# Kernel optimization log

Measured on AMD Instinct MI355X. Metric: run time of the kernel, lower is better.

Reference implementation:

```python
import jax, jax.numpy as jnp
import numpy as np

DIM = 768
NUM_HEADS = 12
HEAD_DIM = DIM // NUM_HEADS
SCALE = HEAD_DIM ** -0.5
B, N = 16, 640  # N = 8*8 + 24*24


def setup_inputs() -> dict:
    key = jax.random.key(0)
    ks = jax.random.split(key, 4)
    x = jax.random.normal(ks[0], (B, N, DIM), dtype=jnp.float32)
    # weights stored input-major: y = x @ W + b (equiv. to torch Linear with W = weight.T)
    qkv_w = jax.random.normal(ks[1], (DIM, 3 * DIM), dtype=jnp.float32) * (DIM ** -0.5)
    qkv_b = jnp.zeros((3 * DIM,), dtype=jnp.float32)
    proj_w = jax.random.normal(ks[2], (DIM, DIM), dtype=jnp.float32) * (DIM ** -0.5)
    proj_b = jnp.zeros((DIM,), dtype=jnp.float32)
    w = jnp.ones((2,), dtype=jnp.float32)
    return {"x": x, "qkv_w": qkv_w, "qkv_b": qkv_b, "proj_w": proj_w,
            "proj_b": proj_b, "w": w, "t_h": 8, "t_w": 8, "s_h": 24, "s_w": 24}


def reference(x, qkv_w, qkv_b, proj_w, proj_b, w, t_h, t_w, s_h, s_w):
    b, n, c = x.shape
    qkv = (x @ qkv_w + qkv_b).reshape(b, n, 3, NUM_HEADS, HEAD_DIM)
    qkv = jnp.transpose(qkv, (2, 0, 3, 1, 4))  # [3, B, H, N, D]
    q, k, v = qkv[0], qkv[1], qkv[2]
    attn = jnp.einsum('bhnd,bhmd->bhnm', q, k) * SCALE  # [B,H,N,N]
    attn0 = jax.nn.softmax(attn, axis=-1)
    attn1 = jnp.square(jax.nn.relu(attn))
    ws = jax.nn.softmax(w)  # exp(w_i)/sum(exp(w)) blend weights
    attn = attn0 * ws[0] + attn1 * ws[1]
    out = jnp.einsum('bhnm,bhmd->bhnd', attn, v)  # [B,H,N,D]
    out = jnp.transpose(out, (0, 2, 1, 3)).reshape(b, n, c)
    return out @ proj_w + proj_b
```

## Files before the change

kernel.cpp:

```cpp
#include <hip/hip_runtime.h>
#include <hip/hip_bf16.h>

typedef __attribute__((ext_vector_type(8))) short short8;
typedef __attribute__((ext_vector_type(4))) float floatx4;
typedef __hip_bfloat16 bf16;

#define DIM 768
#define NH 12
#define HD 64
#define BB 16
#define NN 640
#define BH (BB*NH)
#define MROWS (BB*NN)
#define QKVN (3*DIM)
#define SCALE 0.125f

__device__ __forceinline__ floatx4 mfma16(short8 a, short8 b, floatx4 c) {
    return __builtin_amdgcn_mfma_f32_16x16x32_bf16(a, b, c, 0, 0, 0);
}

__device__ __forceinline__ void async_ld16(const bf16* g, bf16* l) {
    __builtin_amdgcn_global_load_lds(
        (const __attribute__((address_space(1))) void*)g,
        (__attribute__((address_space(3))) void*)l, 16, 0, 0);
}

__device__ __forceinline__ unsigned pack_bf2(float a, float b) {
    union { bf16 h; unsigned short u; } x, y;
    x.h = __float2bfloat16(a); y.h = __float2bfloat16(b);
    return (unsigned)x.u | ((unsigned)y.u << 16);
}


__global__ void cvt_x(const float* __restrict__ x, bf16* __restrict__ xb, int n4) {
    int i = blockIdx.x * blockDim.x + threadIdx.x;
    if (i >= n4) return;
    float4 v = ((const float4*)x)[i];
    bf16* p = xb + (size_t)i * 4;
    p[0] = __float2bfloat16(v.x);
    p[1] = __float2bfloat16(v.y);
    p[2] = __float2bfloat16(v.z);
    p[3] = __float2bfloat16(v.w);
}

__global__ void tr_cvt(const float* __restrict__ src, bf16* __restrict__ dst, int R, int C) {
    __shared__ float tile[32][33];
    int bx = blockIdx.x, by = blockIdx.y;
    int tx = threadIdx.x, ty = threadIdx.y;
    for (int j = 0; j < 4; ++j)
        tile[ty + j*8][tx] = src[(size_t)(by*32 + ty + j*8) * C + bx*32 + tx];
    __syncthreads();
    for (int j = 0; j < 4; ++j)
        dst[(size_t)(bx*32 + ty + j*8) * R + by*32 + tx] = __float2bfloat16(tile[tx][ty + j*8]);
}

__global__ void v_tr(const bf16* __restrict__ qkv, bf16* __restrict__ vT) {
    __shared__ bf16 tile[32][33];
    int bhc = blockIdx.z;
    int b = bhc / NH, h = bhc - b * NH;
    int tt = blockIdx.x, dt = blockIdx.y;
    int tx = threadIdx.x, ty = threadIdx.y;
    for (int j = 0; j < 4; ++j) {
        int tok = tt*32 + ty + j*8;
        tile[ty + j*8][tx] = qkv[(size_t)(b*NN + tok)*QKVN + 2*DIM + h*HD + dt*32 + tx];
    }
    __syncthreads();
    for (int j = 0; j < 4; ++j) {
        int d = dt*32 + ty + j*8;
        vT[((size_t)bhc*HD + d)*NN + tt*32 + tx] = tile[tx][ty + j*8];
    }
}

template<int MODE>
__global__ __launch_bounds__(256) void gemm_bt(
    const bf16* __restrict__ A, const bf16* __restrict__ B, const float* __restrict__ bias,
    int M, int N, int K,
    bf16* __restrict__ outb, float* __restrict__ outf)
{
    __shared__ __align__(16) bf16 As[128*32];
    __shared__ __align__(16) bf16 Bs[128*32];

    const int t = threadIdx.x;
    const int lane = t & 63, wave = t >> 6;
    const int l15 = lane & 15, quad = lane >> 4;
    const int wm = (wave >> 1) * 64, wn = (wave & 1) * 64;
    const int m0 = blockIdx.x * 128, n0 = blockIdx.y * 128;

    floatx4 acc[4][4];
    floatx4 zero = {0.f, 0.f, 0.f, 0.f};
    for (int i = 0; i < 4; ++i)
        for (int j = 0; j < 4; ++j)
            acc[i][j] = zero;

    for (int kk = 0; kk < K; kk += 32) {
        __syncthreads();
        for (int s = 0; s < 2; ++s) {
            int cid = s * 256 + t;
            int row = cid >> 2;
            int c8  = (cid & 3) << 3;
            int lbase = (s * 256 + wave * 64) * 8;
            async_ld16(A + (size_t)(m0 + row) * K + kk + c8, As + lbase);
            async_ld16(B + (size_t)(n0 + row) * K + kk + c8, Bs + lbase);
        }
        __syncthreads();
        short8 af[4], bfv[4];
        for (int fm = 0; fm < 4; ++fm)
            af[fm] = *(const short8*)(As + (wm + fm*16 + l15) * 32 + quad * 8);
        for (int fn = 0; fn < 4; ++fn)
            bfv[fn] = *(const short8*)(Bs + (wn + fn*16 + l15) * 32 + quad * 8);
        for (int fm = 0; fm < 4; ++fm)
            for (int fn = 0; fn < 4; ++fn)
                acc[fm][fn] = mfma16(af[fm], bfv[fn], acc[fm][fn]);
    }

    for (int fm = 0; fm < 4; ++fm) {
        for (int fn = 0; fn < 4; ++fn) {
            int n = n0 + wn + fn*16 + l15;
            float bn = bias[n];
            for (int r = 0; r < 4; ++r) {
                int m = m0 + wm + fm*16 + quad*4 + r;
                float v = acc[fm][fn][r] + bn;
                if (MODE == 0) {
                    if (n < DIM) v *= SCALE;
                    outb[(size_t)m * N + n] = __float2bfloat16(v);
                } else {
                    outf[(size_t)m * N + n] = v;
                }
            }
        }
    }
}

__global__ __launch_bounds__(256) void attn_kernel(
    const bf16* __restrict__ qkv, const bf16* __restrict__ vT,
    const float* __restrict__ w2, bf16* __restrict__ ao)
{
    const int bh = blockIdx.y;
    const int b = bh / NH, h = bh - b * NH;
    const int t = threadIdx.x;
    const int wave = t >> 6;
    const int lane = t & 63;
    const int l15 = lane & 15, quad = lane >> 4;
    const int qrow0 = blockIdx.x * 64 + wave * 16;

    float w0 = w2[0], w1 = w2[1];
    float wmx = fmaxf(w0, w1);
    float e0 = __expf(w0 - wmx), e1 = __expf(w1 - wmx);
    float ws0 = e0 / (e0 + e1), ws1 = 1.0f - ws0;

    __shared__ __align__(16) bf16 Kb[2][32*64];
    __shared__ __align__(16) bf16 Vb[2][64*32];
    __shared__ __align__(16) bf16 Ps[4][16*40];
    __shared__ __align__(16) bf16 Pr[4][16*40];

    const bf16* kg = qkv + (size_t)(b*NN)*QKVN + DIM + h*HD;
    const bf16* vg = vT + (size_t)bh * HD * NN;

    const bf16* qrow = qkv + (size_t)(b*NN + qrow0 + l15) * QKVN + h*HD;
    short8 aq0 = *(const short8*)(qrow + quad*8);
    short8 aq1 = *(const short8*)(qrow + 32 + quad*8);

    const int krow = t >> 3;
    const int kcg  = ((t & 7) ^ (krow & 7)) * 8;
    const int vrow = t >> 2;
    const int vcg  = (t & 3) * 8;

    async_ld16(kg + (size_t)krow * QKVN + kcg, &Kb[0][wave*512]);
    async_ld16(vg + (size_t)vrow * NN + vcg,   &Vb[0][wave*512]);

    floatx4 zero = {0.f, 0.f, 0.f, 0.f};
    floatx4 accS[4], accR[4];
    for (int i = 0; i < 4; ++i) { accS[i] = zero; accR[i] = zero; }
    float lsum = 0.f;

    const int chLo = (quad ^ (l15 & 7)) * 8;
    const int chHi = chLo ^ 32;

    for (int kt = 0; kt < 20; ++kt) {
        const int cur = kt & 1;
        __syncthreads();
        if (kt + 1 < 20) {
            async_ld16(kg + (size_t)((kt+1)*32 + krow) * QKVN + kcg, &Kb[cur^1][wave*512]);
            async_ld16(vg + (size_t)vrow * NN + (kt+1)*32 + vcg,     &Vb[cur^1][wave*512]);
        }

        const bf16* Kc = Kb[cur];
        short8 ak0lo = *(const short8*)(Kc + l15*64 + chLo);
        short8 ak0hi = *(const short8*)(Kc + l15*64 + chHi);
        short8 ak1lo = *(const short8*)(Kc + (16 + l15)*64 + chLo);
        short8 ak1hi = *(const short8*)(Kc + (16 + l15)*64 + chHi);

        const bf16* Vc = Vb[cur];
        short8 bv[4];
        for (int dt = 0; dt < 4; ++dt)
            bv[dt] = *(const short8*)(Vc + (dt*16 + l15)*32 + quad*8);

        floatx4 s0 = zero, s1 = zero;
        s0 = mfma16(ak0lo, aq0, s0);
        s0 = mfma16(ak0hi, aq1, s0);
        s1 = mfma16(ak1lo, aq0, s1);
        s1 = mfma16(ak1hi, aq1, s1);

        float ex0[4], ex1[4], rq0[4], rq1[4];
        for (int r = 0; r < 4; ++r) {
            ex0[r] = __expf(s0[r]);
            ex1[r] = __expf(s1[r]);
            float m0 = fmaxf(s0[r], 0.f), m1 = fmaxf(s1[r], 0.f);
            rq0[r] = m0 * m0;
            rq1[r] = m1 * m1;
            lsum += ex0[r] + ex1[r];
        }

        unsigned* PsW = (unsigned*)&Ps[wave][0];
        unsigned* PrW = (unsigned*)&Pr[wave][0];
        int wb = l15*20 + quad*2;
        PsW[wb]     = pack_bf2(ex0[0], ex0[1]);
        PsW[wb + 1] = pack_bf2(ex0[2], ex0[3]);
        PsW[wb + 8] = pack_bf2(ex1[0], ex1[1]);
        PsW[wb + 9] = pack_bf2(ex1[2], ex1[3]);
        PrW[wb]     = pack_bf2(rq0[0], rq0[1]);
        PrW[wb + 1] = pack_bf2(rq0[2], rq0[3]);
        PrW[wb + 8] = pack_bf2(rq1[0], rq1[1]);
        PrW[wb + 9] = pack_bf2(rq1[2], rq1[3]);

        short8 paS = *(const short8*)(&Ps[wave][l15*40 + quad*8]);
        short8 paR = *(const short8*)(&Pr[wave][l15*40 + quad*8]);

        for (int dt = 0; dt < 4; ++dt) {
            accS[dt] = mfma16(paS, bv[dt], accS[dt]);
            accR[dt] = mfma16(paR, bv[dt], accR[dt]);
        }
    }

    lsum += __shfl_xor(lsum, 16);
    lsum += __shfl_xor(lsum, 32);
    float invq[4];
    for (int r = 0; r < 4; ++r)
        invq[r] = 1.0f / __shfl(lsum, quad*4 + r);

    for (int dt = 0; dt < 4; ++dt) {
        for (int r = 0; r < 4; ++r) {
            float v = ws0 * accS[dt][r] * invq[r] + ws1 * accR[dt][r];
            int tok = qrow0 + quad*4 + r;
            ao[((size_t)(b * NN + tok)) * DIM + h * HD + dt*16 + l15] = __float2bfloat16(v);
        }
    }
}


extern "C" void kernel_launch(void* const* d_in, const int* in_sizes, int n_in,
                              void* d_out, int out_size, void* d_ws, size_t ws_size,
                              hipStream_t stream) {
    const float* x      = (const float*)d_in[0];
    const float* qkv_w  = (const float*)d_in[1];
    const float* qkv_b  = (const float*)d_in[2];
    const float* proj_w = (const float*)d_in[3];
    const float* proj_b = (const float*)d_in[4];
    const float* w2     = (const float*)d_in[5];
    float* out = (float*)d_out;

    bf16* xb   = (bf16*)d_ws;
    bf16* qwT  = xb   + (size_t)MROWS * DIM;
    bf16* pwT  = qwT  + (size_t)QKVN * DIM;
    bf16* qkvb = pwT  + (size_t)DIM * DIM;
    bf16* vT   = qkvb + (size_t)MROWS * QKVN;
    bf16* ao   = xb;

    cvt_x<<<(MROWS * DIM / 4 + 255) / 256, 256, 0, stream>>>(x, xb, MROWS * DIM / 4);
    tr_cvt<<<dim3(QKVN / 32, DIM / 32), dim3(32, 8), 0, stream>>>(qkv_w, qwT, DIM, QKVN);
    tr_cvt<<<dim3(DIM / 32, DIM / 32), dim3(32, 8), 0, stream>>>(proj_w, pwT, DIM, DIM);

    gemm_bt<0><<<dim3(MROWS / 128, QKVN / 128), 256, 0, stream>>>(
        xb, qwT, qkv_b, MROWS, QKVN, DIM, qkvb, nullptr);

    v_tr<<<dim3(NN / 32, HD / 32, BH), dim3(32, 8), 0, stream>>>(qkvb, vT);

    attn_kernel<<<dim3(NN / 64, BH), 256, 0, stream>>>(qkvb, vT, w2, ao);

    gemm_bt<1><<<dim3(MROWS / 128, DIM / 128), 256, 0, stream>>>(
        ao, pwT, proj_b, MROWS, DIM, DIM, nullptr, out);
}
```

Before: 254.2 us.

## Swizzle V tile in LDS, swap attention grid axes, hoist pointer math

XOR-swizzles the 16-byte column groups of the V tile as it is written to shared memory and applies the same swizzle on the read side. This is meant to remove LDS bank conflicts on the V fragment loads. The attention grid is reordered so batch-head is the fast block index, which changes the block scheduling order and how K/V data is shared in L2. Loop-invariant address computations are also hoisted and global pointers are advanced incrementally, adding some register pressure in exchange for fewer integer ops.

```diff
diff --git a/kernel.cpp b/kernel.cpp
--- a/kernel.cpp
+++ b/kernel.cpp
@@ -135,13 +135,13 @@
     const bf16* __restrict__ qkv, const bf16* __restrict__ vT,
     const float* __restrict__ w2, bf16* __restrict__ ao)
 {
-    const int bh = blockIdx.y;
+    const int bh = blockIdx.x;
     const int b = bh / NH, h = bh - b * NH;
     const int t = threadIdx.x;
     const int wave = t >> 6;
     const int lane = t & 63;
     const int l15 = lane & 15, quad = lane >> 4;
-    const int qrow0 = blockIdx.x * 64 + wave * 16;
+    const int qrow0 = blockIdx.y * 64 + wave * 16;
 
     float w0 = w2[0], w1 = w2[1];
     float wmx = fmaxf(w0, w1);
@@ -163,10 +163,13 @@
     const int krow = t >> 3;
     const int kcg  = ((t & 7) ^ (krow & 7)) * 8;
     const int vrow = t >> 2;
-    const int vcg  = (t & 3) * 8;
-
-    async_ld16(kg + (size_t)krow * QKVN + kcg, &Kb[0][wave*512]);
-    async_ld16(vg + (size_t)vrow * NN + vcg,   &Vb[0][wave*512]);
+    const int vcg  = ((t & 3) ^ ((t >> 3) & 3)) * 8;
+
+    const bf16* kgp = kg + (size_t)krow * QKVN + kcg;
+    const bf16* vgp = vg + (size_t)vrow * NN + vcg;
+
+    async_ld16(kgp, &Kb[0][wave*512]);
+    async_ld16(vgp, &Vb[0][wave*512]);
 
     floatx4 zero = {0.f, 0.f, 0.f, 0.f};
     floatx4 accS[4], accR[4];
@@ -175,13 +178,22 @@
 
     const int chLo = (quad ^ (l15 & 7)) * 8;
     const int chHi = chLo ^ 32;
+    const int vslotbase = ((l15 >> 1) & 3);
+
+    unsigned* PsW = (unsigned*)&Ps[wave][0];
+    unsigned* PrW = (unsigned*)&Pr[wave][0];
+    const int wb = l15*20 + quad*2;
+    const bf16* PsR = &Ps[wave][l15*40 + quad*8];
+    const bf16* PrR = &Pr[wave][l15*40 + quad*8];
 
     for (int kt = 0; kt < 20; ++kt) {
         const int cur = kt & 1;
         __syncthreads();
         if (kt + 1 < 20) {
-            async_ld16(kg + (size_t)((kt+1)*32 + krow) * QKVN + kcg, &Kb[cur^1][wave*512]);
-            async_ld16(vg + (size_t)vrow * NN + (kt+1)*32 + vcg,     &Vb[cur^1][wave*512]);
+            kgp += 32 * QKVN;
+            vgp += 32;
+            async_ld16(kgp, &Kb[cur^1][wave*512]);
+            async_ld16(vgp, &Vb[cur^1][wave*512]);
         }
 
         const bf16* Kc = Kb[cur];
@@ -193,7 +205,7 @@
         const bf16* Vc = Vb[cur];
         short8 bv[4];
         for (int dt = 0; dt < 4; ++dt)
-            bv[dt] = *(const short8*)(Vc + (dt*16 + l15)*32 + quad*8);
+            bv[dt] = *(const short8*)(Vc + (dt*16 + l15)*32 + (quad ^ vslotbase)*8);
 
         floatx4 s0 = zero, s1 = zero;
         s0 = mfma16(ak0lo, aq0, s0);
@@ -211,9 +223,6 @@
             lsum += ex0[r] + ex1[r];
         }
 
-        unsigned* PsW = (unsigned*)&Ps[wave][0];
-        unsigned* PrW = (unsigned*)&Pr[wave][0];
-        int wb = l15*20 + quad*2;
         PsW[wb]     = pack_bf2(ex0[0], ex0[1]);
         PsW[wb + 1] = pack_bf2(ex0[2], ex0[3]);
         PsW[wb + 8] = pack_bf2(ex1[0], ex1[1]);
@@ -223,8 +232,8 @@
         PrW[wb + 8] = pack_bf2(rq1[0], rq1[1]);
         PrW[wb + 9] = pack_bf2(rq1[2], rq1[3]);
 
-        short8 paS = *(const short8*)(&Ps[wave][l15*40 + quad*8]);
-        short8 paR = *(const short8*)(&Pr[wave][l15*40 + quad*8]);
+        short8 paS = *(const short8*)PsR;
+        short8 paR = *(const short8*)PrR;
 
         for (int dt = 0; dt < 4; ++dt) {
             accS[dt] = mfma16(paS, bv[dt], accS[dt]);
@@ -275,7 +284,7 @@
 
     v_tr<<<dim3(NN / 32, HD / 32, BH), dim3(32, 8), 0, stream>>>(qkvb, vT);
 
-    attn_kernel<<<dim3(NN / 64, BH), 256, 0, stream>>>(qkvb, vT, w2, ao);
+    attn_kernel<<<dim3(BH, NN / 64), 256, 0, stream>>>(qkvb, vT, w2, ao);
 
     gemm_bt<1><<<dim3(MROWS / 128, DIM / 128), 256, 0, stream>>>(
         ao, pwT, proj_b, MROWS, DIM, DIM, nullptr, out);
```

Result: faster. 248.6 us (-2.2%).
